# Kernel tuning notes

Measured on AMD Instinct MI355X. Metric: run time of the kernel, lower is better.

Reference implementation:

```python
import jax, jax.numpy as jnp
import numpy as np

B, N, T, D = 256, 12, 20, 512
EPS_A = 1e-6          # adjacency row-sum epsilon (matches torch code)
EPS_BN = 1e-5         # BatchNorm2d default eps
DIST_THRESH = 150.0   # pixel distance threshold for graph edges


def setup_inputs() -> dict:
    key = jax.random.key(0)
    ks = jax.random.split(key, 16)
    person_features = jax.random.normal(ks[0], (B, N, T, D), dtype=jnp.float32)
    # bboxes: (x, y, w, h) in pixel coordinates of a 1280x720 frame
    bboxes = jax.random.uniform(ks[1], (B, N, 4), dtype=jnp.float32) \
             * jnp.array([1280.0, 720.0, 120.0, 200.0], dtype=jnp.float32)
    inp = {"person_features": person_features, "bboxes": bboxes}
    # STGCN layer params: 1x1 conv == per-node linear [D_out, D_in], plus BN affine + running stats
    for li in (1, 2):
        k = jax.random.split(ks[1 + li], 6)
        inp[f"W{li}"] = jax.random.normal(k[0], (D, D), dtype=jnp.float32) * (1.0 / np.sqrt(D))
        inp[f"b{li}"] = jax.random.normal(k[1], (D,), dtype=jnp.float32) * 0.01
        inp[f"g{li}"] = jnp.ones((D,), dtype=jnp.float32) + 0.1 * jax.random.normal(k[2], (D,), dtype=jnp.float32)
        inp[f"beta{li}"] = 0.1 * jax.random.normal(k[3], (D,), dtype=jnp.float32)
        inp[f"m{li}"] = 0.1 * jax.random.normal(k[4], (D,), dtype=jnp.float32)
        inp[f"v{li}"] = 0.5 + jax.random.uniform(k[5], (D,), dtype=jnp.float32)
    return inp


def _stgcn(x, A_norm, W, b, g, beta, m, v):
    # x: [B, N, C]; A_norm: [B, N, N] row-normalized adjacency
    # torch: out[c, j] = sum_n x[n, c] * A_norm[n, j]
    xg = jnp.einsum('bnc,bnj->bjc', x, A_norm)           # graph aggregation
    y = xg @ W.T + b                                      # 1x1 conv over channels
    y = g * (y - m) * jax.lax.rsqrt(v + EPS_BN) + beta    # BatchNorm2d (inference)
    return jax.nn.relu(y)


def reference(person_features, bboxes, W1, b1, g1, beta1, m1, v1,
              W2, b2, g2, beta2, m2, v2):
    # box centers: (x + w/2, y + h/2)  -> [B, N, 2]
    centers = jnp.stack([bboxes[..., 0] + bboxes[..., 2] * 0.5,
                         bboxes[..., 1] + bboxes[..., 3] * 0.5], axis=-1)
    # squared pairwise distance (threshold on d^2 avoids sqrt-at-zero); diag d=0<150 -> 1,
    # identical to off-diag threshold + added identity in the torch code.
    diff = centers[:, :, None, :] - centers[:, None, :, :]   # [B, N, N, 2]
    d2 = jnp.sum(diff * diff, axis=-1)                       # [B, N, N]
    A = (d2 < DIST_THRESH * DIST_THRESH).astype(jnp.float32)
    A_norm = A / (jnp.sum(A, axis=-1, keepdims=True) + EPS_A)

    x = person_features[:, :, -1, :]                         # last timestep [B, N, D]
    x = _stgcn(x, A_norm, W1, b1, g1, beta1, m1, v1)
    x = _stgcn(x, A_norm, W2, b2, g2, beta2, m2, v2)
    # write enhanced features back into the last timestep
    return person_features.at[:, :, -1, :].set(x)
```

## Files before the change

kernel.cpp:

```cpp
#include <hip/hip_runtime.h>

#define BB 256
#define NP 12
#define TT 20
#define DD 512
#define EPS_A 1e-6f
#define EPS_BN 1e-5f
#define THR2 (150.0f * 150.0f)
#define APITCH 520
#define CTOTAL 7864320L
#define K2LO   5898240L
#define NCPY1 2048
#define NCPY2 1024

typedef __attribute__((ext_vector_type(8))) short shortx8;
typedef __attribute__((ext_vector_type(4))) float floatx4;

static __device__ __forceinline__ ushort f2bf(float f) {
    unsigned x = __float_as_uint(f);
    return (ushort)((x + 0x7fffu + ((x >> 16) & 1u)) >> 16);
}

static __device__ __forceinline__ void copy_body(int cb, int ncb, int tpb, long lo, long hi,
                                                 const float4* __restrict__ src,
                                                 float4* __restrict__ dst) {
    long stride = (long)ncb * tpb;
    for (long g = lo + (long)cb * tpb + threadIdx.x; g < hi; g += stride) {
        int row = (int)(g >> 7);
        if (row % TT == TT - 1) continue;
        dst[g] = src[g];
    }
}

__global__ __launch_bounds__(256) void k_copyprep(
    const float* __restrict__ W1, const float* __restrict__ W2,
    const float* __restrict__ b1, const float* __restrict__ g1,
    const float* __restrict__ beta1, const float* __restrict__ m1, const float* __restrict__ v1,
    const float* __restrict__ b2, const float* __restrict__ g2,
    const float* __restrict__ beta2, const float* __restrict__ m2, const float* __restrict__ v2,
    float* __restrict__ s1, float* __restrict__ t1, float* __restrict__ s2, float* __restrict__ t2,
    ushort* __restrict__ wb1, ushort* __restrict__ wb2,
    const float4* __restrict__ csrc, float4* __restrict__ cdst) {
    int bid = blockIdx.x, t = threadIdx.x;
    if (bid < 128) {
        int idx = bid * 256 + t;
        #pragma unroll
        for (int k = 0; k < 4; k++) {
            int i = idx + k * 32768;
            float4 f = (i < 65536) ? ((const float4*)W1)[i] : ((const float4*)W2)[i - 65536];
            ushort4 u;
            u.x = f2bf(f.x); u.y = f2bf(f.y); u.z = f2bf(f.z); u.w = f2bf(f.w);
            if (i < 65536) *(ushort4*)(wb1 + (long)i * 4) = u;
            else           *(ushort4*)(wb2 + (long)(i - 65536) * 4) = u;
        }
    } else if (bid == 128) {
        for (int d = t; d < DD; d += 256) {
            float sa = g1[d] * rsqrtf(v1[d] + EPS_BN);
            s1[d] = sa; t1[d] = (b1[d] - m1[d]) * sa + beta1[d];
            float sb = g2[d] * rsqrtf(v2[d] + EPS_BN);
            s2[d] = sb; t2[d] = (b2[d] - m2[d]) * sb + beta2[d];
        }
    } else {
        copy_body(bid - 129, NCPY1, 256, 0L, K2LO, csrc, cdst);
    }
}

template <int LAYER>
static __device__ __forceinline__ void gemm8w(
    int wave, int lane, int b,
    const ushort (*__restrict__ xgl)[APITCH], float (*__restrict__ y1l)[DD],
    const ushort* __restrict__ wb, const float* __restrict__ sv, const float* __restrict__ tv,
    float* __restrict__ outp) {
    int mrow = lane & 15, quad = lane >> 4;
    floatx4 acc[4];
    #pragma unroll
    for (int nt = 0; nt < 4; nt++) acc[nt] = (floatx4){0.f, 0.f, 0.f, 0.f};

    const ushort* wbase = wb + ((long)(wave * 64 + mrow)) * DD + quad * 8;
    #pragma unroll 4
    for (int kc = 0; kc < DD; kc += 32) {
        shortx8 af = *(const shortx8*)&xgl[mrow][kc + quad * 8];
        #pragma unroll
        for (int nt = 0; nt < 4; nt++) {
            shortx8 bf = *(const shortx8*)(wbase + nt * 16 * DD + kc);
            acc[nt] = __builtin_amdgcn_mfma_f32_16x16x32_bf16(af, bf, acc[nt], 0, 0, 0);
        }
    }

    #pragma unroll
    for (int nt = 0; nt < 4; nt++) {
        int d = wave * 64 + nt * 16 + mrow;
        float s = sv[d], tt = tv[d];
        #pragma unroll
        for (int v = 0; v < 4; v++) {
            int m = quad * 4 + v;
            float val = fmaxf(acc[nt][v] * s + tt, 0.f);
            if (m < NP) {
                if (LAYER == 1) y1l[m][d] = val;
                else outp[((long)(b * NP + m) * TT + (TT - 1)) * DD + d] = val;
            }
        }
    }
}

__global__ __launch_bounds__(512, 4) void k_compute(
    const float* __restrict__ pf, const float* __restrict__ bboxes,
    const ushort* __restrict__ wb1, const ushort* __restrict__ wb2,
    const float* __restrict__ s1, const float* __restrict__ t1,
    const float* __restrict__ s2, const float* __restrict__ t2,
    float* __restrict__ out,
    const float4* __restrict__ csrc, float4* __restrict__ cdst) {
    __shared__ float cx[NP], cy[NP], Ash[NP][NP], rinv[NP], at[NP][NP];
    __shared__ __align__(16) ushort xgl[16][APITCH];
    __shared__ float y1l[NP][DD];

    int bid = blockIdx.x, t = threadIdx.x;
    if (bid >= BB) {
        copy_body(bid - BB, NCPY2, 512, K2LO, CTOTAL, csrc, cdst);
        return;
    }

    int b = bid;
    int lane = t & 63, wave = t >> 6;

    if (t < NP) {
        const float* p = bboxes + (b * NP + t) * 4;
        cx[t] = p[0] + 0.5f * p[2];
        cy[t] = p[1] + 0.5f * p[3];
    }
    {
        uint* xz = (uint*)&xgl[NP][0];
        for (int i = t; i < 4 * APITCH / 2; i += 512) xz[i] = 0;
    }
    __syncthreads();
    if (t < NP * NP) {
        int n = t / NP, k = t % NP;
        float dx = cx[n] - cx[k], dy = cy[n] - cy[k];
        Ash[n][k] = (dx * dx + dy * dy < THR2) ? 1.f : 0.f;
    }
    __syncthreads();
    if (t < NP) {
        float s = 0.f;
        #pragma unroll
        for (int k = 0; k < NP; k++) s += Ash[t][k];
        rinv[t] = 1.f / (s + EPS_A);
    }
    __syncthreads();
    if (t < NP * NP) {
        int j = t / NP, n = t % NP;
        at[j][n] = Ash[n][j] * rinv[n];
    }
    __syncthreads();

    for (int c = t; c < DD; c += 512) {
        float xv[NP];
        #pragma unroll
        for (int n = 0; n < NP; n++)
            xv[n] = pf[((long)((b * NP + n) * TT + TT - 1)) * DD + c];
        #pragma unroll
        for (int j = 0; j < NP; j++) {
            float a = 0.f;
            #pragma unroll
            for (int n = 0; n < NP; n++) a += at[j][n] * xv[n];
            xgl[j][c] = f2bf(a);
        }
    }
    __syncthreads();

    gemm8w<1>(wave, lane, b, xgl, y1l, wb1, s1, t1, nullptr);
    __syncthreads();

    for (int c = t; c < DD; c += 512) {
        float xv[NP];
        #pragma unroll
        for (int n = 0; n < NP; n++) xv[n] = y1l[n][c];
        #pragma unroll
        for (int j = 0; j < NP; j++) {
            float a = 0.f;
            #pragma unroll
            for (int n = 0; n < NP; n++) a += at[j][n] * xv[n];
            xgl[j][c] = f2bf(a);
        }
    }
    __syncthreads();

    gemm8w<2>(wave, lane, b, xgl, y1l, wb2, s2, t2, out);
}

extern "C" void kernel_launch(void* const* d_in, const int* in_sizes, int n_in,
                              void* d_out, int out_size, void* d_ws, size_t ws_size,
                              hipStream_t stream) {
    const float* pf = (const float*)d_in[0];
    const float* bboxes = (const float*)d_in[1];
    const float* W1 = (const float*)d_in[2];
    const float* b1 = (const float*)d_in[3];
    const float* g1 = (const float*)d_in[4];
    const float* beta1 = (const float*)d_in[5];
    const float* m1 = (const float*)d_in[6];
    const float* v1 = (const float*)d_in[7];
    const float* W2 = (const float*)d_in[8];
    const float* b2 = (const float*)d_in[9];
    const float* g2 = (const float*)d_in[10];
    const float* beta2 = (const float*)d_in[11];
    const float* m2 = (const float*)d_in[12];
    const float* v2 = (const float*)d_in[13];
    float* out = (float*)d_out;

    float* ws = (float*)d_ws;
    float* s1 = ws;
    float* t1v = ws + 512;
    float* s2 = ws + 1024;
    float* t2v = ws + 1536;
    ushort* wb1 = (ushort*)(ws + 2048);
    ushort* wb2 = wb1 + 262144;

    const float4* csrc = (const float4*)pf;
    float4* cdst = (float4*)out;

    k_copyprep<<<129 + NCPY1, 256, 0, stream>>>(W1, W2, b1, g1, beta1, m1, v1,
                                                b2, g2, beta2, m2, v2,
                                                s1, t1v, s2, t2v, wb1, wb2, csrc, cdst);
    k_compute<<<BB + NCPY2, 512, 0, stream>>>(pf, bboxes, wb1, wb2,
                                              s1, t1v, s2, t2v, out, csrc, cdst);
}
```

Before: 274.1 us.

## Move entire passthrough copy into main kernel with row-indexed wave copies

The bulk copy of non-last timesteps now lives only in the main kernel. Each wave copies four precomputed rows (two float4 loads per lane per row, all issued before the stores), so there is no per-element modulo skip test. The prep kernel shrinks to weight conversion and BN folding. This trades the copy's overlap with weight prep for a single launch that carries more copy blocks alongside the compute blocks.

```diff
diff --git a/kernel.cpp b/kernel.cpp
--- a/kernel.cpp
+++ b/kernel.cpp
@@ -8,10 +8,8 @@
 #define EPS_BN 1e-5f
 #define THR2 (150.0f * 150.0f)
 #define APITCH 520
-#define CTOTAL 7864320L
-#define K2LO   5898240L
-#define NCPY1 2048
-#define NCPY2 1024
+#define NCPY 1824
+#define NSROWS 58368
 
 typedef __attribute__((ext_vector_type(8))) short shortx8;
 typedef __attribute__((ext_vector_type(4))) float floatx4;
@@ -21,47 +19,31 @@
     return (ushort)((x + 0x7fffu + ((x >> 16) & 1u)) >> 16);
 }
 
-static __device__ __forceinline__ void copy_body(int cb, int ncb, int tpb, long lo, long hi,
-                                                 const float4* __restrict__ src,
-                                                 float4* __restrict__ dst) {
-    long stride = (long)ncb * tpb;
-    for (long g = lo + (long)cb * tpb + threadIdx.x; g < hi; g += stride) {
-        int row = (int)(g >> 7);
-        if (row % TT == TT - 1) continue;
-        dst[g] = src[g];
-    }
-}
-
-__global__ __launch_bounds__(256) void k_copyprep(
+__global__ __launch_bounds__(256) void k_prep(
     const float* __restrict__ W1, const float* __restrict__ W2,
     const float* __restrict__ b1, const float* __restrict__ g1,
     const float* __restrict__ beta1, const float* __restrict__ m1, const float* __restrict__ v1,
     const float* __restrict__ b2, const float* __restrict__ g2,
     const float* __restrict__ beta2, const float* __restrict__ m2, const float* __restrict__ v2,
     float* __restrict__ s1, float* __restrict__ t1, float* __restrict__ s2, float* __restrict__ t2,
-    ushort* __restrict__ wb1, ushort* __restrict__ wb2,
-    const float4* __restrict__ csrc, float4* __restrict__ cdst) {
+    ushort* __restrict__ wb1, ushort* __restrict__ wb2) {
     int bid = blockIdx.x, t = threadIdx.x;
-    if (bid < 128) {
-        int idx = bid * 256 + t;
-        #pragma unroll
-        for (int k = 0; k < 4; k++) {
-            int i = idx + k * 32768;
-            float4 f = (i < 65536) ? ((const float4*)W1)[i] : ((const float4*)W2)[i - 65536];
-            ushort4 u;
-            u.x = f2bf(f.x); u.y = f2bf(f.y); u.z = f2bf(f.z); u.w = f2bf(f.w);
-            if (i < 65536) *(ushort4*)(wb1 + (long)i * 4) = u;
-            else           *(ushort4*)(wb2 + (long)(i - 65536) * 4) = u;
-        }
-    } else if (bid == 128) {
+    if (bid < 256) {
+        int i = bid * 256 + t;
+        float4 f1 = ((const float4*)W1)[i];
+        float4 f2 = ((const float4*)W2)[i];
+        ushort4 u1, u2;
+        u1.x = f2bf(f1.x); u1.y = f2bf(f1.y); u1.z = f2bf(f1.z); u1.w = f2bf(f1.w);
+        u2.x = f2bf(f2.x); u2.y = f2bf(f2.y); u2.z = f2bf(f2.z); u2.w = f2bf(f2.w);
+        *(ushort4*)(wb1 + (long)i * 4) = u1;
+        *(ushort4*)(wb2 + (long)i * 4) = u2;
+    } else {
         for (int d = t; d < DD; d += 256) {
             float sa = g1[d] * rsqrtf(v1[d] + EPS_BN);
             s1[d] = sa; t1[d] = (b1[d] - m1[d]) * sa + beta1[d];
             float sb = g2[d] * rsqrtf(v2[d] + EPS_BN);
             s2[d] = sb; t2[d] = (b2[d] - m2[d]) * sb + beta2[d];
         }
-    } else {
-        copy_body(bid - 129, NCPY1, 256, 0L, K2LO, csrc, cdst);
     }
 }
 
@@ -103,25 +85,46 @@
     }
 }
 
-__global__ __launch_bounds__(512, 4) void k_compute(
+__global__ __launch_bounds__(512, 4) void k_main(
     const float* __restrict__ pf, const float* __restrict__ bboxes,
     const ushort* __restrict__ wb1, const ushort* __restrict__ wb2,
     const float* __restrict__ s1, const float* __restrict__ t1,
     const float* __restrict__ s2, const float* __restrict__ t2,
     float* __restrict__ out,
     const float4* __restrict__ csrc, float4* __restrict__ cdst) {
+    int bid = blockIdx.x, t = threadIdx.x;
+    int lane = t & 63, wave = t >> 6;
+
+    if (bid >= BB) {
+        int u = (bid - BB) * 8 + wave;
+        int j0 = u * 4;
+        int base[4];
+        #pragma unroll
+        for (int i = 0; i < 4; i++) {
+            int j = j0 + i;
+            int grp = j / 19;
+            int r = grp * 20 + (j - grp * 19);
+            base[i] = (r << 7) + lane;
+        }
+        float4 v[8];
+        #pragma unroll
+        for (int i = 0; i < 4; i++) {
+            v[2 * i]     = csrc[base[i]];
+            v[2 * i + 1] = csrc[base[i] + 64];
+        }
+        #pragma unroll
+        for (int i = 0; i < 4; i++) {
+            cdst[base[i]]      = v[2 * i];
+            cdst[base[i] + 64] = v[2 * i + 1];
+        }
+        return;
+    }
+
     __shared__ float cx[NP], cy[NP], Ash[NP][NP], rinv[NP], at[NP][NP];
     __shared__ __align__(16) ushort xgl[16][APITCH];
     __shared__ float y1l[NP][DD];
 
-    int bid = blockIdx.x, t = threadIdx.x;
-    if (bid >= BB) {
-        copy_body(bid - BB, NCPY2, 512, K2LO, CTOTAL, csrc, cdst);
-        return;
-    }
-
     int b = bid;
-    int lane = t & 63, wave = t >> 6;
 
     if (t < NP) {
         const float* p = bboxes + (b * NP + t) * 4;
@@ -217,9 +220,9 @@
     const float4* csrc = (const float4*)pf;
     float4* cdst = (float4*)out;
 
-    k_copyprep<<<129 + NCPY1, 256, 0, stream>>>(W1, W2, b1, g1, beta1, m1, v1,
-                                                b2, g2, beta2, m2, v2,
-                                                s1, t1v, s2, t2v, wb1, wb2, csrc, cdst);
-    k_compute<<<BB + NCPY2, 512, 0, stream>>>(pf, bboxes, wb1, wb2,
-                                              s1, t1v, s2, t2v, out, csrc, cdst);
-}
+    k_prep<<<257, 256, 0, stream>>>(W1, W2, b1, g1, beta1, m1, v1,
+                                    b2, g2, beta2, m2, v2,
+                                    s1, t1v, s2, t2v, wb1, wb2);
+    k_main<<<BB + NCPY, 512, 0, stream>>>(pf, bboxes, wb1, wb2,
+                                          s1, t1v, s2, t2v, out, csrc, cdst);
+}
```

After: 266.2 us. -2.9%, faster.

## Move whole passthrough copy into first kernel with unrolled multi-load loop

Applied to the files above, without the earlier changes.

The full input-to-output copy now runs only in the first kernel, so the compute kernel launches just its per-batch blocks. Each copy thread keeps three float4 loads in flight across an unrolled loop, and the per-element last-timestep skip and its modulo test are gone. The last-timestep rows are copied too and later overwritten by the compute kernel, which adds a small amount of extra write traffic. Copy work no longer overlaps the compute kernel, and the weight-conversion blocks are consolidated into fewer blocks.

```diff
diff --git a/kernel.cpp b/kernel.cpp
--- a/kernel.cpp
+++ b/kernel.cpp
@@ -9,9 +9,7 @@
 #define THR2 (150.0f * 150.0f)
 #define APITCH 520
 #define CTOTAL 7864320L
-#define K2LO   5898240L
-#define NCPY1 2048
-#define NCPY2 1024
+#define NCPY 2048
 
 typedef __attribute__((ext_vector_type(8))) short shortx8;
 typedef __attribute__((ext_vector_type(4))) float floatx4;
@@ -21,18 +19,7 @@
     return (ushort)((x + 0x7fffu + ((x >> 16) & 1u)) >> 16);
 }
 
-static __device__ __forceinline__ void copy_body(int cb, int ncb, int tpb, long lo, long hi,
-                                                 const float4* __restrict__ src,
-                                                 float4* __restrict__ dst) {
-    long stride = (long)ncb * tpb;
-    for (long g = lo + (long)cb * tpb + threadIdx.x; g < hi; g += stride) {
-        int row = (int)(g >> 7);
-        if (row % TT == TT - 1) continue;
-        dst[g] = src[g];
-    }
-}
-
-__global__ __launch_bounds__(256) void k_copyprep(
+__global__ __launch_bounds__(256) void k_copyA(
     const float* __restrict__ W1, const float* __restrict__ W2,
     const float* __restrict__ b1, const float* __restrict__ g1,
     const float* __restrict__ beta1, const float* __restrict__ m1, const float* __restrict__ v1,
@@ -42,26 +29,37 @@
     ushort* __restrict__ wb1, ushort* __restrict__ wb2,
     const float4* __restrict__ csrc, float4* __restrict__ cdst) {
     int bid = blockIdx.x, t = threadIdx.x;
-    if (bid < 128) {
+    if (bid >= 65) {
+        const long stride = (long)NCPY * 256;
+        long g = (long)(bid - 65) * 256 + t;
+        #pragma unroll
+        for (int it = 0; it < 5; it++) {
+            float4 a = csrc[g];
+            float4 b = csrc[g + stride];
+            float4 c = csrc[g + 2 * stride];
+            cdst[g] = a;
+            cdst[g + stride] = b;
+            cdst[g + 2 * stride] = c;
+            g += 3 * stride;
+        }
+    } else if (bid < 64) {
         int idx = bid * 256 + t;
         #pragma unroll
-        for (int k = 0; k < 4; k++) {
-            int i = idx + k * 32768;
+        for (int k = 0; k < 8; k++) {
+            int i = idx + k * 16384;
             float4 f = (i < 65536) ? ((const float4*)W1)[i] : ((const float4*)W2)[i - 65536];
             ushort4 u;
             u.x = f2bf(f.x); u.y = f2bf(f.y); u.z = f2bf(f.z); u.w = f2bf(f.w);
             if (i < 65536) *(ushort4*)(wb1 + (long)i * 4) = u;
             else           *(ushort4*)(wb2 + (long)(i - 65536) * 4) = u;
         }
-    } else if (bid == 128) {
+    } else {
         for (int d = t; d < DD; d += 256) {
             float sa = g1[d] * rsqrtf(v1[d] + EPS_BN);
             s1[d] = sa; t1[d] = (b1[d] - m1[d]) * sa + beta1[d];
             float sb = g2[d] * rsqrtf(v2[d] + EPS_BN);
             s2[d] = sb; t2[d] = (b2[d] - m2[d]) * sb + beta2[d];
         }
-    } else {
-        copy_body(bid - 129, NCPY1, 256, 0L, K2LO, csrc, cdst);
     }
 }
 
@@ -108,19 +106,12 @@
     const ushort* __restrict__ wb1, const ushort* __restrict__ wb2,
     const float* __restrict__ s1, const float* __restrict__ t1,
     const float* __restrict__ s2, const float* __restrict__ t2,
-    float* __restrict__ out,
-    const float4* __restrict__ csrc, float4* __restrict__ cdst) {
+    float* __restrict__ out) {
     __shared__ float cx[NP], cy[NP], Ash[NP][NP], rinv[NP], at[NP][NP];
     __shared__ __align__(16) ushort xgl[16][APITCH];
     __shared__ float y1l[NP][DD];
 
-    int bid = blockIdx.x, t = threadIdx.x;
-    if (bid >= BB) {
-        copy_body(bid - BB, NCPY2, 512, K2LO, CTOTAL, csrc, cdst);
-        return;
-    }
-
-    int b = bid;
+    int b = blockIdx.x, t = threadIdx.x;
     int lane = t & 63, wave = t >> 6;
 
     if (t < NP) {
@@ -217,9 +208,9 @@
     const float4* csrc = (const float4*)pf;
     float4* cdst = (float4*)out;
 
-    k_copyprep<<<129 + NCPY1, 256, 0, stream>>>(W1, W2, b1, g1, beta1, m1, v1,
-                                                b2, g2, beta2, m2, v2,
-                                                s1, t1v, s2, t2v, wb1, wb2, csrc, cdst);
-    k_compute<<<BB + NCPY2, 512, 0, stream>>>(pf, bboxes, wb1, wb2,
-                                              s1, t1v, s2, t2v, out, csrc, cdst);
-}
+    k_copyA<<<65 + NCPY, 256, 0, stream>>>(W1, W2, b1, g1, beta1, m1, v1,
+                                           b2, g2, beta2, m2, v2,
+                                           s1, t1v, s2, t2v, wb1, wb2, csrc, cdst);
+    k_compute<<<BB, 512, 0, stream>>>(pf, bboxes, wb1, wb2,
+                                      s1, t1v, s2, t2v, out);
+}
```

Result: slower. 288.8 us (+5.3%).
